# Optimization experiments

Hardware: AMD Instinct MI355X
Metric: run time of the kernel (lower is better)

Reference implementation:

```python
import jax, jax.numpy as jnp
import numpy as np
from jax import lax

DIM, D_STATE, D_CONV, EXPAND = 512, 64, 4, 2
D_INNER = EXPAND * DIM
DT_RANK = (DIM + 15) // 16  # 32
B_SZ, N_LEN = 2, 2048


def setup_inputs() -> dict:
    key = jax.random.key(0)
    ks = jax.random.split(key, 8)
    x = jax.random.normal(ks[0], (B_SZ, N_LEN, DIM), jnp.float32)
    in_proj_w = jax.random.normal(ks[1], (2 * D_INNER, DIM), jnp.float32) * (1.0 / np.sqrt(DIM))
    conv_w = jax.random.normal(ks[2], (D_INNER, 1, D_CONV), jnp.float32) * (1.0 / np.sqrt(D_CONV))
    conv_b = jnp.zeros((D_INNER,), jnp.float32)
    x_proj_w = jax.random.normal(ks[3], (DT_RANK + 2 * D_STATE, D_INNER), jnp.float32) * (1.0 / np.sqrt(D_INNER))
    dt_proj_w = jax.random.normal(ks[4], (D_INNER, DT_RANK), jnp.float32) * (1.0 / np.sqrt(DT_RANK))
    dt_proj_b = jnp.full((D_INNER,), -4.0, jnp.float32) + 0.1 * jax.random.normal(ks[5], (D_INNER,), jnp.float32)
    # S4D-real init: A = -[1..d_state] per channel
    A_log = jnp.log(jnp.broadcast_to(jnp.arange(1, D_STATE + 1, dtype=jnp.float32), (D_INNER, D_STATE)))
    Dp = jnp.ones((D_INNER,), jnp.float32)
    out_proj_w = jax.random.normal(ks[6], (DIM, D_INNER), jnp.float32) * (1.0 / np.sqrt(D_INNER))
    return {"x": x, "norm_w": jnp.ones((DIM,), jnp.float32), "norm_b": jnp.zeros((DIM,), jnp.float32),
            "in_proj_w": in_proj_w, "conv_w": conv_w, "conv_b": conv_b, "x_proj_w": x_proj_w,
            "dt_proj_w": dt_proj_w, "dt_proj_b": dt_proj_b, "A_log": A_log, "D": Dp,
            "out_proj_w": out_proj_w}


def _mamba_layer(x, norm_w, norm_b, in_proj_w, conv_w, conv_b, x_proj_w,
                 dt_proj_w, dt_proj_b, A_log, D, out_proj_w):
    Bsz, N, C = x.shape
    d_inner, d_state = A_log.shape
    dt_rank = dt_proj_w.shape[1]
    d_conv = conv_w.shape[-1]
    # LayerNorm (eps = 1e-5, matches nn.LayerNorm)
    mu = jnp.mean(x, axis=-1, keepdims=True)
    var = jnp.mean(jnp.square(x - mu), axis=-1, keepdims=True)
    xn = (x - mu) * lax.rsqrt(var + 1e-5) * norm_w + norm_b
    # in_proj -> (x, z)
    xz = jnp.einsum('bnc,dc->bnd', xn, in_proj_w)  # (B, N, 2*d_inner)
    xi, z = jnp.split(xz, 2, axis=-1)
    # causal depthwise conv1d along N
    xc = lax.conv_general_dilated(xi.transpose(0, 2, 1), conv_w, window_strides=(1,),
                                  padding=[(d_conv - 1, 0)], feature_group_count=d_inner)
    xi = jax.nn.silu((xc + conv_b[None, :, None]).transpose(0, 2, 1))  # (B, N, d_inner)
    # SSM parameters per token
    x_dbl = jnp.einsum('bnd,rd->bnr', xi, x_proj_w)
    dt, Bs, Cs = jnp.split(x_dbl, [dt_rank, dt_rank + d_state], axis=-1)
    dt = jax.nn.softplus(jnp.einsum('bnr,dr->bnd', dt, dt_proj_w) + dt_proj_b)  # (B, N, d_inner)
    A = -jnp.exp(A_log)  # (d_inner, d_state)

    def step(h, inp):
        dt_t, B_t, C_t, u_t = inp  # (B,d), (B,s), (B,s), (B,d)
        dA = jnp.exp(dt_t[:, :, None] * A)                       # (B, d_inner, d_state)
        dBu = (dt_t * u_t)[:, :, None] * B_t[:, None, :]
        h = dA * h + dBu
        y = jnp.einsum('bds,bs->bd', h, C_t)
        return h, y

    h0 = jnp.zeros((Bsz, d_inner, d_state), x.dtype)
    xs = (dt.transpose(1, 0, 2), Bs.transpose(1, 0, 2), Cs.transpose(1, 0, 2), xi.transpose(1, 0, 2))
    _, ys = lax.scan(step, h0, xs)                               # (N, B, d_inner)
    y = ys.transpose(1, 0, 2) + xi * D                           # skip term D*u
    y = y * jax.nn.silu(z)                                       # gating
    return jnp.einsum('bnd,cd->bnc', y, out_proj_w)


def reference(x, norm_w, norm_b, in_proj_w, conv_w, conv_b, x_proj_w,
              dt_proj_w, dt_proj_b, A_log, D, out_proj_w):
    return _mamba_layer(x, norm_w, norm_b, in_proj_w, conv_w, conv_b, x_proj_w,
                        dt_proj_w, dt_proj_b, A_log, D, out_proj_w)
```

## Files before the change

kernel.cpp:

```cpp
#include <hip/hip_runtime.h>

#define D_MODEL 512
#define DINNER  1024
#define DSTATE  64
#define DTRANK  32
#define BSZ     2
#define NLEN    2048
#define NROWS   (BSZ*NLEN)
#define XDBL_W  (DTRANK + 2*DSTATE)

typedef __attribute__((ext_vector_type(8))) short  bf16x8;
typedef __attribute__((ext_vector_type(4))) float  f32x4;
typedef __attribute__((ext_vector_type(8))) unsigned short u16x8;

__device__ __forceinline__ unsigned int rne16(float f) {
    unsigned int u = __float_as_uint(f);
    return (u + 0x7fffu + ((u >> 16) & 1)) >> 16;
}
__device__ __forceinline__ float fsilu(float x) {
    return x / (1.f + __builtin_amdgcn_exp2f(-x * 1.44269504f));
}

__device__ __forceinline__ void pack_frag(const float* __restrict__ src,
        unsigned short* __restrict__ dst, int R, int RT, int K,
        int gid, int lane) {
    const int kt = gid / RT, rt = gid - kt * RT;
    const int row = (rt << 4) + (lane & 15);
    const int KTK = K >> 5;
    u16x8 hi = {}, lo = {};
    if (row < R) {
        const float* s = src + (size_t)row * K + kt * 32 + ((lane >> 4) << 3);
        float4 f0 = *(const float4*)s;
        float4 f1 = *(const float4*)(s + 4);
        float ff[8] = {f0.x,f0.y,f0.z,f0.w,f1.x,f1.y,f1.z,f1.w};
        #pragma unroll
        for (int j = 0; j < 8; ++j) {
            unsigned int hb = rne16(ff[j]);
            hi[j] = (unsigned short)hb;
            lo[j] = (unsigned short)rne16(ff[j] - __uint_as_float(hb << 16));
        }
    }
    *(u16x8*)(dst + ((size_t)kt * RT + rt) * 512 + lane * 8) = hi;
    *(u16x8*)(dst + ((size_t)(kt + KTK) * RT + rt) * 512 + lane * 8) = lo;
}

__global__ __launch_bounds__(256) void prologue(const float* __restrict__ x,
        const float* __restrict__ nw, const float* __restrict__ nb,
        const float* __restrict__ in_w, const float* __restrict__ x_w,
        const float* __restrict__ out_w, unsigned short* __restrict__ Ap,
        unsigned short* __restrict__ BpIn, unsigned short* __restrict__ BpX,
        unsigned short* __restrict__ BpOut, float* __restrict__ xdbl) {
    __shared__ float xs[16][516];
    const int bid = blockIdx.x;
    const int wid = threadIdx.x >> 6, lane = threadIdx.x & 63;
    if (bid < 256) {
        const int rt = bid;
        const float4* wp = (const float4*)nw;
        const float4* bp = (const float4*)nb;
        const float4 w0 = wp[lane], w1 = wp[lane + 64];
        const float4 b0 = bp[lane], b1 = bp[lane + 64];
        #pragma unroll
        for (int pq = 0; pq < 4; ++pq) {
            const int r = (wid << 2) + pq;
            const int row = (rt << 4) + r;
            const float4* xp = (const float4*)(x + (size_t)row * D_MODEL);
            float4 v0 = xp[lane], v1 = xp[lane + 64];
            float s = v0.x + v0.y + v0.z + v0.w + v1.x + v1.y + v1.z + v1.w;
            float q = v0.x*v0.x + v0.y*v0.y + v0.z*v0.z + v0.w*v0.w
                    + v1.x*v1.x + v1.y*v1.y + v1.z*v1.z + v1.w*v1.w;
            #pragma unroll
            for (int m = 32; m; m >>= 1) { s += __shfl_xor(s, m); q += __shfl_xor(q, m); }
            const float mean = s * (1.f / D_MODEL);
            const float var  = q * (1.f / D_MODEL) - mean * mean;
            const float rstd = rsqrtf(var + 1e-5f);
            float4 o0, o1;
            o0.x = (v0.x - mean) * rstd * w0.x + b0.x;
            o0.y = (v0.y - mean) * rstd * w0.y + b0.y;
            o0.z = (v0.z - mean) * rstd * w0.z + b0.z;
            o0.w = (v0.w - mean) * rstd * w0.w + b0.w;
            o1.x = (v1.x - mean) * rstd * w1.x + b1.x;
            o1.y = (v1.y - mean) * rstd * w1.y + b1.y;
            o1.z = (v1.z - mean) * rstd * w1.z + b1.z;
            o1.w = (v1.w - mean) * rstd * w1.w + b1.w;
            *(float4*)&xs[r][lane << 2] = o0;
            *(float4*)&xs[r][256 + (lane << 2)] = o1;
        }
        __syncthreads();
        const int r = lane & 15;
        const int cq = (lane >> 4) << 3;
        #pragma unroll
        for (int q = 0; q < 4; ++q) {
            const int kt = (wid << 2) + q;
            const int c0 = (kt << 5) + cq;
            float4 f0 = *(const float4*)&xs[r][c0];
            float4 f1 = *(const float4*)&xs[r][c0 + 4];
            float ff[8] = {f0.x,f0.y,f0.z,f0.w,f1.x,f1.y,f1.z,f1.w};
            u16x8 hi, lo;
            #pragma unroll
            for (int j = 0; j < 8; ++j) {
                unsigned int hb = rne16(ff[j]);
                hi[j] = (unsigned short)hb;
                lo[j] = (unsigned short)rne16(ff[j] - __uint_as_float(hb << 16));
            }
            *(u16x8*)(Ap + ((size_t)kt * 256 + rt) * 512 + lane * 8) = hi;
            *(u16x8*)(Ap + ((size_t)(kt + 16) * 256 + rt) * 512 + lane * 8) = lo;
        }
    } else if (bid < 768) {
        pack_frag(in_w, BpIn, 2048, 128, 512, (bid - 256) * 4 + wid, lane);
    } else if (bid < 896) {
        pack_frag(x_w, BpX, 160, 16, 1024, (bid - 768) * 4 + wid, lane);
    } else if (bid < 1152) {
        pack_frag(out_w, BpOut, 512, 32, 1024, (bid - 896) * 4 + wid, lane);
    } else {
        float* p = xdbl + (size_t)(bid - 1152) * 4096 + threadIdx.x * 4;
        const float4 z4 = make_float4(0.f, 0.f, 0.f, 0.f);
        *(float4*)p = z4; *(float4*)(p + 1024) = z4;
        *(float4*)(p + 2048) = z4; *(float4*)(p + 3072) = z4;
    }
}

template<int BM, int BN, int WR, int WC, bool ATOMIC>
__global__ __launch_bounds__(256) void gemm_mfma(
        const unsigned short* __restrict__ Ap, const unsigned short* __restrict__ Bp,
        int M, int N, int K, int cols3, int terms,
        float* __restrict__ out0, float* __restrict__ out1, int split) {
    constexpr int MI = BM / (WR * 16);
    constexpr int NI = BN / (WC * 16);
    constexpr int APASS = BM / 64;
    constexpr int BPASS = BN / 64;
    __shared__ __align__(16) unsigned short sA[2 * BM * 32];
    __shared__ __align__(16) unsigned short sB[2 * BN * 32];
    const int tid = threadIdx.x;
    const int wid = tid >> 6, lane = tid & 63;
    const int wr = wid / WC, wc = wid % WC;
    const int m0 = blockIdx.y * BM, n0 = blockIdx.x * BN;
    if (ATOMIC && blockIdx.z > 0 && n0 >= cols3) return;
    const int MT = M >> 4, NT = N >> 4;
    const int KTK = K >> 5;
    const int KTv = ATOMIC ? KTK : ((n0 < cols3) ? terms * KTK : KTK);
    const int aoff = (ATOMIC && blockIdx.z == 1) ? KTK : 0;
    const int boff = (ATOMIC && blockIdx.z == 2) ? KTK : 0;
    f32x4 acc[MI][NI] = {};
    for (int kt2 = 0; kt2 < KTv; kt2 += 2) {
        __syncthreads();
        #pragma unroll
        for (int tt = 0; tt < 2; ++tt) {
            const int kt = kt2 + tt;
            int a_kt, b_kt;
            if (ATOMIC) { a_kt = kt + aoff; b_kt = kt + boff; }
            else { a_kt = (kt < 2 * KTK) ? kt : kt - 2 * KTK;
                   b_kt = (kt < KTK) ? kt : kt - KTK; }
            const char* gA = (const char*)(Ap + ((size_t)a_kt * MT + (m0 >> 4)) * 512);
            const char* gB = (const char*)(Bp + ((size_t)b_kt * NT + (n0 >> 4)) * 512);
            #pragma unroll
            for (int p = 0; p < APASS; ++p)
                __builtin_amdgcn_global_load_lds(
                    (const __attribute__((address_space(1))) void*)(gA + p * 4096 + tid * 16),
                    (__attribute__((address_space(3))) void*)((char*)sA + tt * BM * 64 + p * 4096 + tid * 16),
                    16, 0, 0);
            #pragma unroll
            for (int p = 0; p < BPASS; ++p)
                __builtin_amdgcn_global_load_lds(
                    (const __attribute__((address_space(1))) void*)(gB + p * 4096 + tid * 16),
                    (__attribute__((address_space(3))) void*)((char*)sB + tt * BN * 64 + p * 4096 + tid * 16),
                    16, 0, 0);
        }
        __syncthreads();
        #pragma unroll
        for (int tt = 0; tt < 2; ++tt) {
            bf16x8 af[MI], bfr[NI];
            #pragma unroll
            for (int mi = 0; mi < MI; ++mi)
                af[mi] = *(const bf16x8*)((const char*)sA + tt*BM*64 + (wr*MI + mi)*1024 + lane*16);
            #pragma unroll
            for (int ni = 0; ni < NI; ++ni)
                bfr[ni] = *(const bf16x8*)((const char*)sB + tt*BN*64 + (wc*NI + ni)*1024 + lane*16);
            #pragma unroll
            for (int mi = 0; mi < MI; ++mi)
                #pragma unroll
                for (int ni = 0; ni < NI; ++ni)
                    acc[mi][ni] = __builtin_amdgcn_mfma_f32_16x16x32_bf16(
                        af[mi], bfr[ni], acc[mi][ni], 0, 0, 0);
        }
    }
    #pragma unroll
    for (int mi = 0; mi < MI; ++mi) {
        #pragma unroll
        for (int ni = 0; ni < NI; ++ni) {
            const int col = n0 + (wc*NI + ni)*16 + (lane & 15);
            const int rb_ = m0 + (wr*MI + mi)*16 + ((lane >> 4) << 2);
            if (col < split) {
                #pragma unroll
                for (int r = 0; r < 4; ++r) {
                    if (ATOMIC) atomicAdd(&out0[(size_t)(rb_ + r) * split + col], acc[mi][ni][r]);
                    else        out0[(size_t)(rb_ + r) * split + col] = acc[mi][ni][r];
                }
            } else if (!ATOMIC && out1 != nullptr) {
                #pragma unroll
                for (int r = 0; r < 4; ++r)
                    out1[(size_t)(rb_ + r) * (N - split) + (col - split)] = acc[mi][ni][r];
            }
        }
    }
}

__global__ __launch_bounds__(256) void conv_pack(const float* __restrict__ xr,
        const float* __restrict__ cw, const float* __restrict__ cb,
        float* __restrict__ xi, unsigned short* __restrict__ Ap) {
    const int wid = threadIdx.x >> 6, lane = threadIdx.x & 63;
    const int gid = (blockIdx.x << 2) + wid;
    const int kt = gid >> 8, rt = gid & 255;
    const int row = (rt << 4) + (lane & 15);
    const int n = row & (NLEN - 1);
    const int d0 = (kt << 5) + ((lane >> 4) << 3);
    const float* base = xr + (size_t)row * DINNER + d0;
    const float4 z4 = make_float4(0.f, 0.f, 0.f, 0.f);
    float4 c0 = *(const float4*)base,          c1 = *(const float4*)(base + 4);
    float4 a0 = (n >= 1) ? *(const float4*)(base - DINNER)     : z4;
    float4 a1 = (n >= 1) ? *(const float4*)(base - DINNER + 4) : z4;
    float4 b0 = (n >= 2) ? *(const float4*)(base - 2*DINNER)     : z4;
    float4 b1 = (n >= 2) ? *(const float4*)(base - 2*DINNER + 4) : z4;
    float4 e0 = (n >= 3) ? *(const float4*)(base - 3*DINNER)     : z4;
    float4 e1 = (n >= 3) ? *(const float4*)(base - 3*DINNER + 4) : z4;
    float cur[8] = {c0.x,c0.y,c0.z,c0.w,c1.x,c1.y,c1.z,c1.w};
    float p1[8]  = {a0.x,a0.y,a0.z,a0.w,a1.x,a1.y,a1.z,a1.w};
    float p2[8]  = {b0.x,b0.y,b0.z,b0.w,b1.x,b1.y,b1.z,b1.w};
    float p3[8]  = {e0.x,e0.y,e0.z,e0.w,e1.x,e1.y,e1.z,e1.w};
    float o[8];
    u16x8 hi, lo;
    #pragma unroll
    for (int j = 0; j < 8; ++j) {
        const float4 wv = *(const float4*)(cw + (d0 + j) * 4);
        float a = cb[d0 + j];
        a = fmaf(wv.w, cur[j], a);
        a = fmaf(wv.z, p1[j], a);
        a = fmaf(wv.y, p2[j], a);
        a = fmaf(wv.x, p3[j], a);
        o[j] = fsilu(a);
        unsigned int hb = rne16(o[j]);
        hi[j] = (unsigned short)hb;
        lo[j] = (unsigned short)rne16(o[j] - __uint_as_float(hb << 16));
    }
    float* xo = xi + (size_t)row * DINNER + d0;
    *(float4*)xo = make_float4(o[0], o[1], o[2], o[3]);
    *(float4*)(xo + 4) = make_float4(o[4], o[5], o[6], o[7]);
    *(u16x8*)(Ap + ((size_t)kt * 256 + rt) * 512 + lane * 8) = hi;
    *(u16x8*)(Ap + ((size_t)(kt + 32) * 256 + rt) * 512 + lane * 8) = lo;
}

__global__ __launch_bounds__(256) void dtdu_kernel(const float* __restrict__ xdbl,
        const float* __restrict__ W, const float* __restrict__ bias,
        const float* __restrict__ u, float* __restrict__ dtT,
        float* __restrict__ duT, unsigned int* __restrict__ bc) {
    if (blockIdx.x >= 1024) {
        const int row0 = (blockIdx.x - 1024) << 6;
        #pragma unroll
        for (int k = 0; k < 16; ++k) {
            const int g = threadIdx.x * 16 + k;
            const int lr = g >> 6, s = g & 63;
            const int row = row0 + lr;
            const float* src = xdbl + (size_t)row * XDBL_W + DTRANK + s;
            bc[(size_t)(row >> 2) * 256 + s * 4 + (row & 3)] =
                rne16(src[0]) | (rne16(src[DSTATE]) << 16);
        }
        return;
    }
    __shared__ float sdtr[64][33];
    __shared__ float sW[64][33];
    __shared__ float tt[64][65];
    const int nb = blockIdx.x & 63, db = blockIdx.x >> 6;
    const int row0 = nb << 6, d0 = db << 6;
    const int i = threadIdx.x >> 2, kq = (threadIdx.x & 3) << 3;
    {
        const float* s = xdbl + (size_t)(row0 + i) * XDBL_W + kq;
        *(float4*)&sdtr[i][kq]     = *(const float4*)s;
        *(float4*)&sdtr[i][kq + 4] = *(const float4*)(s + 4);
        const float* wsrc = W + (size_t)(d0 + i) * DTRANK + kq;
        *(float4*)&sW[i][kq]     = *(const float4*)wsrc;
        *(float4*)&sW[i][kq + 4] = *(const float4*)(wsrc + 4);
    }
    __syncthreads();
    const int i4 = (threadIdx.x >> 4) << 2;
    const int j4 = (threadIdx.x & 15) << 2;
    float dtv[4][4], duv[4][4];
    {
        float acc[4][4] = {};
        #pragma unroll
        for (int k = 0; k < DTRANK; ++k) {
            float a[4]  = {sdtr[i4][k], sdtr[i4+1][k], sdtr[i4+2][k], sdtr[i4+3][k]};
            float bb[4] = {sW[j4][k], sW[j4+1][k], sW[j4+2][k], sW[j4+3][k]};
            #pragma unroll
            for (int ii = 0; ii < 4; ++ii)
                #pragma unroll
                for (int jj = 0; jj < 4; ++jj)
                    acc[ii][jj] = fmaf(a[ii], bb[jj], acc[ii][jj]);
        }
        float4 bv = *(const float4*)(bias + d0 + j4);
        float bb4[4] = {bv.x, bv.y, bv.z, bv.w};
        #pragma unroll
        for (int ii = 0; ii < 4; ++ii) {
            float4 uv = *(const float4*)(u + (size_t)(row0 + i4 + ii) * DINNER + d0 + j4);
            float uu[4] = {uv.x, uv.y, uv.z, uv.w};
            #pragma unroll
            for (int jj = 0; jj < 4; ++jj) {
                float z = acc[ii][jj] + bb4[jj];
                float dt = (z > 20.f) ? z : log1pf(expf(z));
                dtv[ii][jj] = dt;
                duv[ii][jj] = dt * uu[jj];
            }
        }
    }
    const int b = row0 >> 11;
    const int n0 = row0 & (NLEN - 1);
    const int jt = threadIdx.x >> 2, iq = (threadIdx.x & 3) << 4;
    float* dstD = dtT + ((size_t)(b * DINNER + d0 + jt)) * NLEN + n0 + iq;
    float* dstU = duT + ((size_t)(b * DINNER + d0 + jt)) * NLEN + n0 + iq;
    #pragma unroll
    for (int ii = 0; ii < 4; ++ii)
        #pragma unroll
        for (int jj = 0; jj < 4; ++jj)
            tt[i4 + ii][j4 + jj] = dtv[ii][jj];
    __syncthreads();
    #pragma unroll
    for (int r = 0; r < 4; ++r) {
        float4 o = make_float4(tt[iq+4*r+0][jt], tt[iq+4*r+1][jt],
                               tt[iq+4*r+2][jt], tt[iq+4*r+3][jt]);
        *(float4*)(dstD + 4*r) = o;
    }
    __syncthreads();
    #pragma unroll
    for (int ii = 0; ii < 4; ++ii)
        #pragma unroll
        for (int jj = 0; jj < 4; ++jj)
            tt[i4 + ii][j4 + jj] = duv[ii][jj];
    __syncthreads();
    #pragma unroll
    for (int r = 0; r < 4; ++r) {
        float4 o = make_float4(tt[iq+4*r+0][jt], tt[iq+4*r+1][jt],
                               tt[iq+4*r+2][jt], tt[iq+4*r+3][jt]);
        *(float4*)(dstU + 4*r) = o;
    }
}

__global__ __launch_bounds__(256) void scan_kernel(const float* __restrict__ dtT,
        const float* __restrict__ duT, const unsigned int* __restrict__ bc,
        const float* __restrict__ A_log, float* __restrict__ yt) {
    __shared__ float p[4][32][65];
    __shared__ float2 dd[4][64];
    const int wid = threadIdx.x >> 6;
    const int w = (blockIdx.x << 2) + wid;
    const int lane = threadIdx.x & 63;
    const int b = w >> 10, d = w & (DINNER - 1);
    const float* dtp = dtT + (size_t)w * NLEN;
    const float* dup = duT + (size_t)w * NLEN;
    const unsigned int* bcb = bc + (size_t)b * NLEN * 64 + lane * 4;
    float* yp = yt + (size_t)w * NLEN;
    const float kA = -__builtin_amdgcn_exp2f(A_log[d * DSTATE + lane] * 1.44269504f)
                     * 1.44269504f;
    float (*pw)[65] = p[wid];
    float2* ddw = dd[wid];
    const int rn = lane & 31, rs = (lane >> 5) << 5;
    float h = 0.f;
    float gdt = dtp[lane], gdu = dup[lane];
    for (int n0 = 0; n0 < NLEN; n0 += 64) {
        ddw[lane] = make_float2(gdt, gdu);
        if (n0 + 64 < NLEN) { gdt = dtp[n0 + 64 + lane]; gdu = dup[n0 + 64 + lane]; }
        const unsigned int* bq = bcb + (size_t)n0 * 64;
        #pragma unroll
        for (int half = 0; half < 2; ++half) {
            const unsigned int* bh  = bq + (half << 3) * 256;
            const unsigned int* bh2 = bh + 4 * 256;
            #pragma unroll
            for (int g = 0; g < 8; ++g) {
                const uint4 qv = (g < 4) ? *(const uint4*)(bh + g * 256)
                                         : *(const uint4*)(bh2 + (g - 4) * 256);
                #pragma unroll
                for (int e = 0; e < 4; ++e) {
                    const int j = (g << 2) + e;
                    const unsigned int q = (e == 0) ? qv.x : (e == 1) ? qv.y
                                         : (e == 2) ? qv.z : qv.w;
                    const float2 v = ddw[(half << 5) + j];
                    const float Bv = __uint_as_float(q << 16);
                    const float Cv = __uint_as_float(q & 0xffff0000u);
                    h = fmaf(__builtin_amdgcn_exp2f(kA * v.x), h, v.y * Bv);
                    pw[j][lane] = h * Cv;
                }
            }
            float y0 = 0.f, y1 = 0.f, y2 = 0.f, y3 = 0.f;
            #pragma unroll
            for (int i = 0; i < 32; i += 4) {
                y0 += pw[rn][rs + i];
                y1 += pw[rn][rs + i + 1];
                y2 += pw[rn][rs + i + 2];
                y3 += pw[rn][rs + i + 3];
            }
            float y = (y0 + y1) + (y2 + y3);
            y += __shfl_xor(y, 32);
            if (lane < 32) yp[n0 + (half << 5) + rn] = y;
        }
    }
}

__global__ __launch_bounds__(256) void gate_pack(const float* __restrict__ yt,
        const float* __restrict__ xi, const float* __restrict__ z,
        const float* __restrict__ Dv, unsigned short* __restrict__ Ap) {
    const int wid = threadIdx.x >> 6, lane = threadIdx.x & 63;
    const int gid = (blockIdx.x << 2) + wid;
    const int kt = gid >> 8, rt = gid & 255;
    const int row = (rt << 4) + (lane & 15);
    const int n = row & (NLEN - 1), b = row >> 11;
    const int d0 = (kt << 5) + ((lane >> 4) << 3);
    const float* ytp = yt + ((size_t)(b * DINNER + d0)) * NLEN + n;
    const float* xp = xi + (size_t)row * DINNER + d0;
    const float* zp = z  + (size_t)row * DINNER + d0;
    float4 x0 = *(const float4*)xp, x1 = *(const float4*)(xp + 4);
    float4 z0 = *(const float4*)zp, z1 = *(const float4*)(zp + 4);
    float4 D0 = *(const float4*)(Dv + d0), D1 = *(const float4*)(Dv + d0 + 4);
    float xv[8] = {x0.x,x0.y,x0.z,x0.w,x1.x,x1.y,x1.z,x1.w};
    float zv[8] = {z0.x,z0.y,z0.z,z0.w,z1.x,z1.y,z1.z,z1.w};
    float dv[8] = {D0.x,D0.y,D0.z,D0.w,D1.x,D1.y,D1.z,D1.w};
    u16x8 hi, lo;
    #pragma unroll
    for (int j = 0; j < 8; ++j) {
        const float yv = ytp[(size_t)j * NLEN];
        const float g = fmaf(xv[j], dv[j], yv) * fsilu(zv[j]);
        unsigned int hb = rne16(g);
        hi[j] = (unsigned short)hb;
        lo[j] = (unsigned short)rne16(g - __uint_as_float(hb << 16));
    }
    *(u16x8*)(Ap + ((size_t)kt * 256 + rt) * 512 + lane * 8) = hi;
    *(u16x8*)(Ap + ((size_t)(kt + 32) * 256 + rt) * 512 + lane * 8) = lo;
}

extern "C" void kernel_launch(void* const* d_in, const int* in_sizes, int n_in,
                              void* d_out, int out_size, void* d_ws, size_t ws_size,
                              hipStream_t stream) {
    const float* x         = (const float*)d_in[0];
    const float* norm_w    = (const float*)d_in[1];
    const float* norm_b    = (const float*)d_in[2];
    const float* in_proj_w = (const float*)d_in[3];
    const float* conv_w    = (const float*)d_in[4];
    const float* conv_b    = (const float*)d_in[5];
    const float* x_proj_w  = (const float*)d_in[6];
    const float* dt_proj_w = (const float*)d_in[7];
    const float* dt_proj_b = (const float*)d_in[8];
    const float* A_log     = (const float*)d_in[9];
    const float* Dvec      = (const float*)d_in[10];
    const float* out_proj_w= (const float*)d_in[11];
    float* out = (float*)d_out;
    float* ws  = (float*)d_ws;

    const size_t M1 = (size_t)1024 * 1024;
    float* dtT    = ws;
    float* xi_duT = ws + 4*M1;
    float* zbuf   = ws + 8*M1;
    float* xibuf  = ws + 12*M1;
    float* xdbl   = ws + 16*M1;
    float* ytbuf  = ws + 17*M1;
    unsigned short* Apack = (unsigned short*)(ws + 21*M1);
    unsigned int*   bcbuf = (unsigned int*)(ws + 21*M1);
    unsigned short* BpIn  = (unsigned short*)(ws + 26*M1);
    unsigned short* BpX   = (unsigned short*)(ws + 27*M1);
    unsigned short* BpOut = (unsigned short*)(ws + 27*M1 + 512*1024);

    prologue<<<1312, 256, 0, stream>>>(x, norm_w, norm_b, in_proj_w, x_proj_w,
        out_proj_w, Apack, BpIn, BpX, BpOut, xdbl);

    gemm_mfma<128,128,2,2,false><<<dim3(16, 32), 256, 0, stream>>>(
        Apack, BpIn, 4096, 2048, 512, DINNER, 2,
        xi_duT, zbuf, DINNER);

    conv_pack<<<(32 * 256) / 4, 256, 0, stream>>>(
        xi_duT, conv_w, conv_b, xibuf, Apack);

    gemm_mfma<128,64,2,2,true><<<dim3(3, 32, 2), 256, 0, stream>>>(
        Apack, BpX, 4096, 256, 1024, 64, 0,
        xdbl, nullptr, XDBL_W);

    dtdu_kernel<<<1024 + 64, 256, 0, stream>>>(xdbl, dt_proj_w, dt_proj_b,
        xibuf, dtT, xi_duT, bcbuf);
    scan_kernel<<<(BSZ * DINNER) / 4, 256, 0, stream>>>(
        dtT, xi_duT, bcbuf, A_log, ytbuf);

    gate_pack<<<(32 * 256) / 4, 256, 0, stream>>>(
        ytbuf, xibuf, zbuf, Dvec, Apack);

    gemm_mfma<64,64,2,2,false><<<dim3(8, 64), 256, 0, stream>>>(
        Apack, BpOut, 4096, 512, 1024, 512, 2,
        out, nullptr, D_MODEL);
}
```

Baseline: 256.8 us.

## Split-K the x_proj GEMM four ways and store scan output as bf16

The atomic x_proj GEMM now splits K into four chunks per term, growing the grid depth from 2 to 8 so more blocks run in parallel, with each block accumulating its partial product via atomics. The bf16 B-term for the low half was also dropped (boff removed), leaving only hi*hi and lo*hi products. Separately, the scan kernel writes y as bf16 instead of fp32 and gate_pack reads bf16, halving that intermediate traffic. Risks are extra atomic contention and lower precision in y before gating.

```diff
diff --git a/kernel.cpp b/kernel.cpp
--- a/kernel.cpp
+++ b/kernel.cpp
@@ -122,7 +122,7 @@
 template<int BM, int BN, int WR, int WC, bool ATOMIC>
 __global__ __launch_bounds__(256) void gemm_mfma(
         const unsigned short* __restrict__ Ap, const unsigned short* __restrict__ Bp,
-        int M, int N, int K, int cols3, int terms,
+        int M, int N, int K, int cols3, int tk,
         float* __restrict__ out0, float* __restrict__ out1, int split) {
     constexpr int MI = BM / (WR * 16);
     constexpr int NI = BN / (WC * 16);
@@ -134,12 +134,18 @@
     const int wid = tid >> 6, lane = tid & 63;
     const int wr = wid / WC, wc = wid % WC;
     const int m0 = blockIdx.y * BM, n0 = blockIdx.x * BN;
-    if (ATOMIC && blockIdx.z > 0 && n0 >= cols3) return;
     const int MT = M >> 4, NT = N >> 4;
     const int KTK = K >> 5;
-    const int KTv = ATOMIC ? KTK : ((n0 < cols3) ? terms * KTK : KTK);
-    const int aoff = (ATOMIC && blockIdx.z == 1) ? KTK : 0;
-    const int boff = (ATOMIC && blockIdx.z == 2) ? KTK : 0;
+    int KTv, kbase = 0, aoff = 0;
+    if (ATOMIC) {
+        const int term = blockIdx.z & 1;
+        if (term && n0 >= cols3) return;
+        KTv = KTK / tk;
+        kbase = (blockIdx.z >> 1) * KTv;
+        aoff = term ? KTK : 0;
+    } else {
+        KTv = (n0 < cols3) ? tk * KTK : KTK;
+    }
     f32x4 acc[MI][NI] = {};
     for (int kt2 = 0; kt2 < KTv; kt2 += 2) {
         __syncthreads();
@@ -147,7 +153,7 @@
         for (int tt = 0; tt < 2; ++tt) {
             const int kt = kt2 + tt;
             int a_kt, b_kt;
-            if (ATOMIC) { a_kt = kt + aoff; b_kt = kt + boff; }
+            if (ATOMIC) { a_kt = kbase + kt + aoff; b_kt = kbase + kt; }
             else { a_kt = (kt < 2 * KTK) ? kt : kt - 2 * KTK;
                    b_kt = (kt < KTK) ? kt : kt - KTK; }
             const char* gA = (const char*)(Ap + ((size_t)a_kt * MT + (m0 >> 4)) * 512);
@@ -344,7 +350,7 @@
 
 __global__ __launch_bounds__(256) void scan_kernel(const float* __restrict__ dtT,
         const float* __restrict__ duT, const unsigned int* __restrict__ bc,
-        const float* __restrict__ A_log, float* __restrict__ yt) {
+        const float* __restrict__ A_log, unsigned short* __restrict__ ytb) {
     __shared__ float p[4][32][65];
     __shared__ float2 dd[4][64];
     const int wid = threadIdx.x >> 6;
@@ -354,7 +360,7 @@
     const float* dtp = dtT + (size_t)w * NLEN;
     const float* dup = duT + (size_t)w * NLEN;
     const unsigned int* bcb = bc + (size_t)b * NLEN * 64 + lane * 4;
-    float* yp = yt + (size_t)w * NLEN;
+    unsigned short* yp = ytb + (size_t)w * NLEN;
     const float kA = -__builtin_amdgcn_exp2f(A_log[d * DSTATE + lane] * 1.44269504f)
                      * 1.44269504f;
     float (*pw)[65] = p[wid];
@@ -396,12 +402,12 @@
             }
             float y = (y0 + y1) + (y2 + y3);
             y += __shfl_xor(y, 32);
-            if (lane < 32) yp[n0 + (half << 5) + rn] = y;
-        }
-    }
-}
-
-__global__ __launch_bounds__(256) void gate_pack(const float* __restrict__ yt,
+            if (lane < 32) yp[n0 + (half << 5) + rn] = (unsigned short)rne16(y);
+        }
+    }
+}
+
+__global__ __launch_bounds__(256) void gate_pack(const unsigned short* __restrict__ ytb,
         const float* __restrict__ xi, const float* __restrict__ z,
         const float* __restrict__ Dv, unsigned short* __restrict__ Ap) {
     const int wid = threadIdx.x >> 6, lane = threadIdx.x & 63;
@@ -410,7 +416,7 @@
     const int row = (rt << 4) + (lane & 15);
     const int n = row & (NLEN - 1), b = row >> 11;
     const int d0 = (kt << 5) + ((lane >> 4) << 3);
-    const float* ytp = yt + ((size_t)(b * DINNER + d0)) * NLEN + n;
+    const unsigned short* ytp = ytb + ((size_t)(b * DINNER + d0)) * NLEN + n;
     const float* xp = xi + (size_t)row * DINNER + d0;
     const float* zp = z  + (size_t)row * DINNER + d0;
     float4 x0 = *(const float4*)xp, x1 = *(const float4*)(xp + 4);
@@ -422,7 +428,7 @@
     u16x8 hi, lo;
     #pragma unroll
     for (int j = 0; j < 8; ++j) {
-        const float yv = ytp[(size_t)j * NLEN];
+        const float yv = __uint_as_float((unsigned int)ytp[(size_t)j * NLEN] << 16);
         const float g = fmaf(xv[j], dv[j], yv) * fsilu(zv[j]);
         unsigned int hb = rne16(g);
         hi[j] = (unsigned short)hb;
@@ -456,7 +462,7 @@
     float* zbuf   = ws + 8*M1;
     float* xibuf  = ws + 12*M1;
     float* xdbl   = ws + 16*M1;
-    float* ytbuf  = ws + 17*M1;
+    unsigned short* ytbuf = (unsigned short*)(ws + 17*M1);
     unsigned short* Apack = (unsigned short*)(ws + 21*M1);
     unsigned int*   bcbuf = (unsigned int*)(ws + 21*M1);
     unsigned short* BpIn  = (unsigned short*)(ws + 26*M1);
@@ -473,8 +479,8 @@
     conv_pack<<<(32 * 256) / 4, 256, 0, stream>>>(
         xi_duT, conv_w, conv_b, xibuf, Apack);
 
-    gemm_mfma<128,64,2,2,true><<<dim3(3, 32, 2), 256, 0, stream>>>(
-        Apack, BpX, 4096, 256, 1024, 64, 0,
+    gemm_mfma<128,64,2,2,true><<<dim3(3, 32, 8), 256, 0, stream>>>(
+        Apack, BpX, 4096, 256, 1024, 64, 4,
         xdbl, nullptr, XDBL_W);
 
     dtdu_kernel<<<1024 + 64, 256, 0, stream>>>(xdbl, dt_proj_w, dt_proj_b,
```

Result: no change. 256.8 us (+0.0%).
